# Kernel tuning notes

Measured on AMD Instinct MI355X. Metric: run time of the kernel, lower is better.

Reference implementation:

```python
import jax, jax.numpy as jnp
import numpy as np

N_NODES = 100000
N_EDGES = 1000000
IN_CH = 312
HID = 256
OUT = 256


def _sage_conv(x, src, dst, W_l, b_l, W_r, num_nodes):
    # PyG SAGEConv (mean aggr): out = mean_{j in N(i)} x_j @ W_l + b_l + x_i @ W_r
    msg = x[src]                                             # [E, C] gather
    agg = jax.ops.segment_sum(msg, dst, num_segments=num_nodes)  # [N, C]
    deg = jax.ops.segment_sum(jnp.ones((src.shape[0],), dtype=x.dtype), dst,
                              num_segments=num_nodes)        # [N]
    mean = agg / jnp.maximum(deg, 1.0)[:, None]
    return mean @ W_l + b_l + x @ W_r


def setup_inputs() -> dict:
    key = jax.random.key(0)
    ks = jax.random.split(key, 8)
    x = jax.random.normal(ks[0], (N_NODES, IN_CH), dtype=jnp.float32)
    edge_index = jax.random.randint(ks[1], (2, N_EDGES), 0, N_NODES, dtype=jnp.int64)
    s1 = 1.0 / np.sqrt(IN_CH)
    s2 = 1.0 / np.sqrt(HID)
    W1_l = jax.random.normal(ks[2], (IN_CH, HID), dtype=jnp.float32) * s1
    b1 = jnp.zeros((HID,), dtype=jnp.float32)
    W1_r = jax.random.normal(ks[3], (IN_CH, HID), dtype=jnp.float32) * s1
    W2_l = jax.random.normal(ks[4], (HID, OUT), dtype=jnp.float32) * s2
    b2 = jnp.zeros((OUT,), dtype=jnp.float32)
    W2_r = jax.random.normal(ks[5], (HID, OUT), dtype=jnp.float32) * s2
    return {"x": x, "edge_index": edge_index, "W1_l": W1_l, "b1": b1,
            "W1_r": W1_r, "W2_l": W2_l, "b2": b2, "W2_r": W2_r}


def reference(x, edge_index, W1_l, b1, W1_r, W2_l, b2, W2_r):
    src, dst = edge_index[0], edge_index[1]
    n = x.shape[0]
    h = _sage_conv(x, src, dst, W1_l, b1, W1_r, n)
    h = jax.nn.relu(h)
    out = _sage_conv(h, src, dst, W2_l, b2, W2_r, n)
    return out
```

## Files before the change

kernel.cpp:

```cpp
#include <hip/hip_runtime.h>
#include <hip/hip_bf16.h>
#include <cstdint>
#include <cstddef>

#define IN_CH 312
#define HID 256

typedef __attribute__((ext_vector_type(8))) short bf16x8;
typedef __attribute__((ext_vector_type(4))) float f32x4;
typedef __attribute__((ext_vector_type(8))) unsigned short ushort8;

__device__ __forceinline__ unsigned short f2bf(float f) {
    union { float f; unsigned u; } v; v.f = f;
    const unsigned r = v.u + 0x7FFFu + ((v.u >> 16) & 1u);
    return (unsigned short)(r >> 16);
}
__device__ __forceinline__ float bf2f(unsigned short s) {
    union { unsigned u; float f; } v; v.u = (unsigned)s << 16;
    return v.f;
}
__device__ __forceinline__ void gload_lds16(const void* g, void* l) {
    __builtin_amdgcn_global_load_lds(
        (const __attribute__((address_space(1))) void*)g,
        (__attribute__((address_space(3))) void*)l, 16, 0, 0);
}

__global__ void detect_idx_kernel(const void* __restrict__ ei, int* __restrict__ flag) {
    if (blockIdx.x == 0 && threadIdx.x == 0) {
        const int* p = (const int*)ei;
        int ok = 1;
        for (int i = 0; i < 64; ++i) ok &= (p[2 * i + 1] == 0);
        *flag = ok;
    }
}
__device__ __forceinline__ long long load_idx(const void* ei, long long i, bool is64) {
    return is64 ? ((const long long*)ei)[i] : (long long)((const int*)ei)[i];
}

__global__ void hist_kernel(const void* __restrict__ ei, const int* __restrict__ flag,
                            int* __restrict__ cnt, int E) {
    const int i = blockIdx.x * blockDim.x + threadIdx.x;
    if (i >= E) return;
    const bool is64 = (*flag != 0);
    atomicAdd(&cnt[load_idx(ei, (long long)E + i, is64)], 1);
}

__global__ void offsets_kernel(const int* __restrict__ cnt, int* __restrict__ counter,
                               int* __restrict__ beg, int* __restrict__ cur, int n) {
    const int i = blockIdx.x * blockDim.x + threadIdx.x;
    if (i >= n) return;
    const int b = atomicAdd(counter, cnt[i]);
    beg[i] = b;
    cur[i] = b;
}

__global__ void fill_kernel(const void* __restrict__ ei, const int* __restrict__ flag,
                            int* __restrict__ cur, int* __restrict__ col, int E) {
    const int i = blockIdx.x * blockDim.x + threadIdx.x;
    if (i >= E) return;
    const bool is64 = (*flag != 0);
    const long long s = load_idx(ei, i, is64);
    const long long d = load_idx(ei, (long long)E + i, is64);
    col[atomicAdd(&cur[d], 1)] = (int)s;
}

__global__ void convert_x_kernel(const float* __restrict__ x, unsigned short* __restrict__ xb,
                                 int N) {
    const int tid = blockIdx.x * blockDim.x + threadIdx.x;
    if (tid >= N * 40) return;
    const int row = tid / 40;
    const int c8 = (tid % 40) * 8;
    ushort8 o;
    if (c8 < IN_CH) {
        const float4 v0 = *(const float4*)(x + (size_t)row * IN_CH + c8);
        const float4 v1 = *(const float4*)(x + (size_t)row * IN_CH + c8 + 4);
        o[0] = f2bf(v0.x); o[1] = f2bf(v0.y); o[2] = f2bf(v0.z); o[3] = f2bf(v0.w);
        o[4] = f2bf(v1.x); o[5] = f2bf(v1.y); o[6] = f2bf(v1.z); o[7] = f2bf(v1.w);
    } else {
        o = (ushort8)0;
    }
    *(ushort8*)(xb + (size_t)row * 320 + c8) = o;
}

__global__ void convert_w_kernel(const float* __restrict__ Wl, const float* __restrict__ Wr,
                                 unsigned short* __restrict__ wt, int K, int Kpad) {
    const int tid = blockIdx.x * blockDim.x + threadIdx.x;
    if (tid >= 512 * Kpad) return;
    const int c = tid / Kpad;
    const int k = tid % Kpad;
    float v = 0.f;
    if (k < K) v = (c < 256) ? Wl[(size_t)k * 256 + c] : Wr[(size_t)k * 256 + (c - 256)];
    wt[(size_t)c * Kpad + k] = f2bf(v);
}

template <int KPAD, bool ZBF16>
__global__ __launch_bounds__(256) void mfma_gemm_kernel(
    const unsigned short* __restrict__ A,
    const unsigned short* __restrict__ WT,
    const float* __restrict__ bias,
    unsigned short* __restrict__ Y,
    void* __restrict__ Z,
    int M)
{
    __shared__ short a_lds[128 * 64];
    __shared__ short b_lds[128 * 64];

    const int lane = threadIdx.x & 63;
    const int wid  = threadIdx.x >> 6;
    const int wr = wid >> 1, wc = wid & 1;
    const int r0 = blockIdx.x * 128;
    const int c0 = blockIdx.y * 128;

    f32x4 acc[4][4];
    #pragma unroll
    for (int i = 0; i < 4; ++i)
        #pragma unroll
        for (int j = 0; j < 4; ++j) acc[i][j] = (f32x4)0.f;

    const int ldrow  = lane >> 3;
    const int schunk = (lane & 7) ^ ldrow;

    for (int kb = 0; kb < KPAD; kb += 64) {
        __syncthreads();
        #pragma unroll
        for (int j = 0; j < 4; ++j) {
            const int ld = wid * 4 + j;
            const int trow = ld * 8 + ldrow;
            const int agr = min(r0 + trow, M - 1);
            gload_lds16(A + (size_t)agr * KPAD + kb + schunk * 8,
                        (char*)a_lds + ld * 1024);
            gload_lds16(WT + (size_t)(c0 + trow) * KPAD + kb + schunk * 8,
                        (char*)b_lds + ld * 1024);
        }
        __syncthreads();

        #pragma unroll
        for (int ks = 0; ks < 2; ++ks) {
            bf16x8 af[4], bg[4];
            #pragma unroll
            for (int f = 0; f < 4; ++f) {
                const int arow = wr * 64 + f * 16 + (lane & 15);
                const int ach  = (ks * 4 + (lane >> 4)) ^ (arow & 7);
                af[f] = *(const bf16x8*)((const char*)a_lds + arow * 128 + ach * 16);
                const int brow = wc * 64 + f * 16 + (lane & 15);
                const int bch  = (ks * 4 + (lane >> 4)) ^ (brow & 7);
                bg[f] = *(const bf16x8*)((const char*)b_lds + brow * 128 + bch * 16);
            }
            #pragma unroll
            for (int fm = 0; fm < 4; ++fm)
                #pragma unroll
                for (int fn = 0; fn < 4; ++fn)
                    acc[fm][fn] = __builtin_amdgcn_mfma_f32_16x16x32_bf16(
                        af[fm], bg[fn], acc[fm][fn], 0, 0, 0);
        }
    }

    const int rbase = r0 + wr * 64 + (lane >> 4) * 4;
    const int cbase = c0 + wc * 64 + (lane & 15);
    if (c0 < 256) {
        #pragma unroll
        for (int fm = 0; fm < 4; ++fm)
            #pragma unroll
            for (int fn = 0; fn < 4; ++fn) {
                const int gc = cbase + fn * 16;
                #pragma unroll
                for (int r = 0; r < 4; ++r) {
                    const int gr = rbase + fm * 16 + r;
                    if (gr < M) Y[(size_t)gr * 256 + gc] = f2bf(acc[fm][fn][r]);
                }
            }
    } else {
        #pragma unroll
        for (int fn = 0; fn < 4; ++fn) {
            const int gc = cbase + fn * 16 - 256;
            const float bv = bias[gc];
            #pragma unroll
            for (int fm = 0; fm < 4; ++fm)
                #pragma unroll
                for (int r = 0; r < 4; ++r) {
                    const int gr = rbase + fm * 16 + r;
                    if (gr < M) {
                        const float zv = acc[fm][fn][r] + bv;
                        if (ZBF16)
                            ((unsigned short*)Z)[(size_t)gr * 256 + gc] = f2bf(zv);
                        else
                            ((float*)Z)[(size_t)gr * 256 + gc] = zv;
                    }
                }
        }
    }
}

template <bool LAYER1>
__global__ void gather_agg_kernel(const unsigned short* __restrict__ Y,
                                  const int* __restrict__ beg_arr,
                                  const int* __restrict__ cnt,
                                  const int* __restrict__ col,
                                  const void* __restrict__ Z,
                                  void* __restrict__ OUT, int N)
{
    const long long gw = ((long long)blockIdx.x * blockDim.x + threadIdx.x) >> 6;
    if (gw >= N) return;
    const int w = (int)gw;
    const int lane = threadIdx.x & 63;
    const int c4 = lane * 4;
    const int beg = beg_arr[w];
    const int deg = cnt[w];
    const int end = beg + deg;

    float4 acc = make_float4(0.f, 0.f, 0.f, 0.f);
    int e = beg;
    for (; e + 1 < end; e += 2) {
        const int s0 = col[e], s1 = col[e + 1];
        const ushort4 v0 = *(const ushort4*)(Y + (size_t)s0 * 256 + c4);
        const ushort4 v1 = *(const ushort4*)(Y + (size_t)s1 * 256 + c4);
        acc.x += bf2f(v0.x) + bf2f(v1.x);
        acc.y += bf2f(v0.y) + bf2f(v1.y);
        acc.z += bf2f(v0.z) + bf2f(v1.z);
        acc.w += bf2f(v0.w) + bf2f(v1.w);
    }
    if (e < end) {
        const ushort4 v0 = *(const ushort4*)(Y + (size_t)col[e] * 256 + c4);
        acc.x += bf2f(v0.x); acc.y += bf2f(v0.y);
        acc.z += bf2f(v0.z); acc.w += bf2f(v0.w);
    }

    const float inv = 1.0f / fmaxf((float)deg, 1.0f);
    float4 z;
    if (LAYER1) {
        const ushort4 zb = *(const ushort4*)((const unsigned short*)Z + (size_t)w * 256 + c4);
        z = make_float4(bf2f(zb.x), bf2f(zb.y), bf2f(zb.z), bf2f(zb.w));
    } else {
        z = *(const float4*)((const float*)Z + (size_t)w * 256 + c4);
    }
    float4 o;
    o.x = acc.x * inv + z.x;
    o.y = acc.y * inv + z.y;
    o.z = acc.z * inv + z.z;
    o.w = acc.w * inv + z.w;
    if (LAYER1) {
        o.x = fmaxf(o.x, 0.f); o.y = fmaxf(o.y, 0.f);
        o.z = fmaxf(o.z, 0.f); o.w = fmaxf(o.w, 0.f);
        ushort4 ob;
        ob.x = f2bf(o.x); ob.y = f2bf(o.y); ob.z = f2bf(o.z); ob.w = f2bf(o.w);
        *(ushort4*)((unsigned short*)OUT + (size_t)w * 256 + c4) = ob;
    } else {
        *(float4*)((float*)OUT + (size_t)w * 256 + c4) = o;
    }
}

extern "C" void kernel_launch(void* const* d_in, const int* in_sizes, int n_in,
                              void* d_out, int out_size, void* d_ws, size_t ws_size,
                              hipStream_t stream) {
    const float* x   = (const float*)d_in[0];
    const void*  ei  = d_in[1];
    const float* W1l = (const float*)d_in[2];
    const float* b1  = (const float*)d_in[3];
    const float* W1r = (const float*)d_in[4];
    const float* W2l = (const float*)d_in[5];
    const float* b2  = (const float*)d_in[6];
    const float* W2r = (const float*)d_in[7];

    const int N = in_sizes[0] / IN_CH;
    const int E = in_sizes[1] / 2;

    char* ws = (char*)d_ws;
    size_t off = 0;
    auto alloc = [&](size_t bytes) {
        void* p = ws + off;
        off = (off + bytes + 255) & ~(size_t)255;
        return p;
    };
    int* flag    = (int*)alloc(4);
    int* cnt     = (int*)alloc((size_t)(N + 1) * 4);
    int* counter = cnt + N;
    int* beg     = (int*)alloc((size_t)N * 4);
    int* cur     = (int*)alloc((size_t)N * 4);
    int* col     = (int*)alloc((size_t)E * 4);
    unsigned short* wt1 = (unsigned short*)alloc((size_t)512 * 320 * 2);
    unsigned short* wt2 = (unsigned short*)alloc((size_t)512 * 256 * 2);
    unsigned short* bufA = (unsigned short*)alloc((size_t)N * 320 * 2);
    unsigned short* y    = (unsigned short*)alloc((size_t)N * 256 * 2);

    float* out = (float*)d_out;
    unsigned short* z1 = (unsigned short*)d_out;

    hipMemsetAsync(cnt, 0, (size_t)(N + 1) * 4, stream);
    detect_idx_kernel<<<1, 64, 0, stream>>>(ei, flag);
    hist_kernel<<<(E + 255) / 256, 256, 0, stream>>>(ei, flag, cnt, E);
    offsets_kernel<<<(N + 255) / 256, 256, 0, stream>>>(cnt, counter, beg, cur, N);
    fill_kernel<<<(E + 255) / 256, 256, 0, stream>>>(ei, flag, cur, col, E);

    convert_x_kernel<<<(N * 40 + 255) / 256, 256, 0, stream>>>(x, bufA, N);
    convert_w_kernel<<<(512 * 320 + 255) / 256, 256, 0, stream>>>(W1l, W1r, wt1, IN_CH, 320);
    convert_w_kernel<<<(512 * 256 + 255) / 256, 256, 0, stream>>>(W2l, W2r, wt2, HID, 256);

    const dim3 ggrid((N + 127) / 128, 4);

    mfma_gemm_kernel<320, true><<<ggrid, 256, 0, stream>>>(bufA, wt1, b1, y, z1, N);
    gather_agg_kernel<true><<<(N + 3) / 4, 256, 0, stream>>>(y, beg, cnt, col, z1, bufA, N);

    mfma_gemm_kernel<256, false><<<ggrid, 256, 0, stream>>>(bufA, wt2, b2, y, out, N);
    gather_agg_kernel<false><<<(N + 3) / 4, 256, 0, stream>>>(y, beg, cnt, col, out, out, N);
}
```

Before: 535.7 us.

## Fuse fp32-to-bf16 conversion of x into GEMM and use full-width 64-row tiles

Removes the separate convert_x kernel: the first GEMM now loads fp32 x directly, converts it to bf16 in registers and writes swizzled bf16 into LDS. The GEMM tile is restructured so each block computes 64 rows by all 512 output columns, with each wave owning 128 columns. A is therefore read once instead of four times across column blocks. The trade-off is 64KB of B staged in LDS per block, more accumulators per wave (lower occupancy), and fp32 A loads that go through registers instead of direct-to-LDS loads.

```diff
diff --git a/kernel.cpp b/kernel.cpp
--- a/kernel.cpp
+++ b/kernel.cpp
@@ -8,7 +8,6 @@
 
 typedef __attribute__((ext_vector_type(8))) short bf16x8;
 typedef __attribute__((ext_vector_type(4))) float f32x4;
-typedef __attribute__((ext_vector_type(8))) unsigned short ushort8;
 
 __device__ __forceinline__ unsigned short f2bf(float f) {
     union { float f; unsigned u; } v; v.f = f;
@@ -62,24 +61,6 @@
     const long long s = load_idx(ei, i, is64);
     const long long d = load_idx(ei, (long long)E + i, is64);
     col[atomicAdd(&cur[d], 1)] = (int)s;
-}
-
-__global__ void convert_x_kernel(const float* __restrict__ x, unsigned short* __restrict__ xb,
-                                 int N) {
-    const int tid = blockIdx.x * blockDim.x + threadIdx.x;
-    if (tid >= N * 40) return;
-    const int row = tid / 40;
-    const int c8 = (tid % 40) * 8;
-    ushort8 o;
-    if (c8 < IN_CH) {
-        const float4 v0 = *(const float4*)(x + (size_t)row * IN_CH + c8);
-        const float4 v1 = *(const float4*)(x + (size_t)row * IN_CH + c8 + 4);
-        o[0] = f2bf(v0.x); o[1] = f2bf(v0.y); o[2] = f2bf(v0.z); o[3] = f2bf(v0.w);
-        o[4] = f2bf(v1.x); o[5] = f2bf(v1.y); o[6] = f2bf(v1.z); o[7] = f2bf(v1.w);
-    } else {
-        o = (ushort8)0;
-    }
-    *(ushort8*)(xb + (size_t)row * 320 + c8) = o;
 }
 
 __global__ void convert_w_kernel(const float* __restrict__ Wl, const float* __restrict__ Wr,
@@ -93,29 +74,27 @@
     wt[(size_t)c * Kpad + k] = f2bf(v);
 }
 
-template <int KPAD, bool ZBF16>
+template <int KPAD, bool AFP32, bool ZBF16>
 __global__ __launch_bounds__(256) void mfma_gemm_kernel(
-    const unsigned short* __restrict__ A,
+    const void* __restrict__ Avoid,
     const unsigned short* __restrict__ WT,
     const float* __restrict__ bias,
     unsigned short* __restrict__ Y,
     void* __restrict__ Z,
     int M)
 {
-    __shared__ short a_lds[128 * 64];
-    __shared__ short b_lds[128 * 64];
+    __shared__ short a_lds[64 * 64];
+    __shared__ short b_lds[512 * 64];
 
     const int lane = threadIdx.x & 63;
     const int wid  = threadIdx.x >> 6;
-    const int wr = wid >> 1, wc = wid & 1;
-    const int r0 = blockIdx.x * 128;
-    const int c0 = blockIdx.y * 128;
-
-    f32x4 acc[4][4];
+    const int r0   = blockIdx.x * 64;
+
+    f32x4 acc[4][8];
     #pragma unroll
     for (int i = 0; i < 4; ++i)
         #pragma unroll
-        for (int j = 0; j < 4; ++j) acc[i][j] = (f32x4)0.f;
+        for (int j = 0; j < 8; ++j) acc[i][j] = (f32x4)0.f;
 
     const int ldrow  = lane >> 3;
     const int schunk = (lane & 7) ^ ldrow;
@@ -123,46 +102,79 @@
     for (int kb = 0; kb < KPAD; kb += 64) {
         __syncthreads();
         #pragma unroll
-        for (int j = 0; j < 4; ++j) {
-            const int ld = wid * 4 + j;
+        for (int j = 0; j < 16; ++j) {
+            const int ld = wid * 16 + j;
             const int trow = ld * 8 + ldrow;
-            const int agr = min(r0 + trow, M - 1);
-            gload_lds16(A + (size_t)agr * KPAD + kb + schunk * 8,
-                        (char*)a_lds + ld * 1024);
-            gload_lds16(WT + (size_t)(c0 + trow) * KPAD + kb + schunk * 8,
+            gload_lds16(WT + (size_t)trow * KPAD + kb + schunk * 8,
                         (char*)b_lds + ld * 1024);
         }
+        if (AFP32) {
+            const float* A = (const float*)Avoid;
+            float4 v[4];
+            #pragma unroll
+            for (int it = 0; it < 4; ++it) {
+                const int idx = (int)threadIdx.x + it * 256;
+                const int row = idx >> 4, q = idx & 15;
+                const int gr = min(r0 + row, M - 1);
+                const int gk = kb + q * 4;
+                v[it] = (gk < IN_CH) ? *(const float4*)(A + (size_t)gr * IN_CH + gk)
+                                     : make_float4(0.f, 0.f, 0.f, 0.f);
+            }
+            #pragma unroll
+            for (int it = 0; it < 4; ++it) {
+                const int idx = (int)threadIdx.x + it * 256;
+                const int row = idx >> 4, q = idx & 15;
+                ushort4 b;
+                b.x = f2bf(v[it].x); b.y = f2bf(v[it].y);
+                b.z = f2bf(v[it].z); b.w = f2bf(v[it].w);
+                const int byte = row * 128 + (((q >> 1) ^ (row & 7)) * 16) + (q & 1) * 8;
+                *(ushort4*)((char*)a_lds + byte) = b;
+            }
+        } else {
+            const unsigned short* A = (const unsigned short*)Avoid;
+            #pragma unroll
+            for (int j = 0; j < 2; ++j) {
+                const int ld = wid * 2 + j;
+                const int trow = ld * 8 + ldrow;
+                const int gr = min(r0 + trow, M - 1);
+                gload_lds16(A + (size_t)gr * KPAD + kb + schunk * 8,
+                            (char*)a_lds + ld * 1024);
+            }
+        }
         __syncthreads();
 
         #pragma unroll
         for (int ks = 0; ks < 2; ++ks) {
-            bf16x8 af[4], bg[4];
+            bf16x8 af[4], bg[8];
             #pragma unroll
             for (int f = 0; f < 4; ++f) {
-                const int arow = wr * 64 + f * 16 + (lane & 15);
+                const int arow = f * 16 + (lane & 15);
                 const int ach  = (ks * 4 + (lane >> 4)) ^ (arow & 7);
                 af[f] = *(const bf16x8*)((const char*)a_lds + arow * 128 + ach * 16);
-                const int brow = wc * 64 + f * 16 + (lane & 15);
+            }
+            #pragma unroll
+            for (int f = 0; f < 8; ++f) {
+                const int brow = wid * 128 + f * 16 + (lane & 15);
                 const int bch  = (ks * 4 + (lane >> 4)) ^ (brow & 7);
                 bg[f] = *(const bf16x8*)((const char*)b_lds + brow * 128 + bch * 16);
             }
             #pragma unroll
             for (int fm = 0; fm < 4; ++fm)
                 #pragma unroll
-                for (int fn = 0; fn < 4; ++fn)
+                for (int fn = 0; fn < 8; ++fn)
                     acc[fm][fn] = __builtin_amdgcn_mfma_f32_16x16x32_bf16(
                         af[fm], bg[fn], acc[fm][fn], 0, 0, 0);
         }
     }
 
-    const int rbase = r0 + wr * 64 + (lane >> 4) * 4;
-    const int cbase = c0 + wc * 64 + (lane & 15);
-    if (c0 < 256) {
+    const int rbase = r0 + (lane >> 4) * 4;
+    const int cwave = wid * 128 + (lane & 15);
+    if (wid < 2) {
         #pragma unroll
         for (int fm = 0; fm < 4; ++fm)
             #pragma unroll
-            for (int fn = 0; fn < 4; ++fn) {
-                const int gc = cbase + fn * 16;
+            for (int fn = 0; fn < 8; ++fn) {
+                const int gc = cwave + fn * 16;
                 #pragma unroll
                 for (int r = 0; r < 4; ++r) {
                     const int gr = rbase + fm * 16 + r;
@@ -171,8 +183,8 @@
             }
     } else {
         #pragma unroll
-        for (int fn = 0; fn < 4; ++fn) {
-            const int gc = cbase + fn * 16 - 256;
+        for (int fn = 0; fn < 8; ++fn) {
+            const int gc = cwave + fn * 16 - 256;
             const float bv = bias[gc];
             #pragma unroll
             for (int fm = 0; fm < 4; ++fm)
@@ -279,8 +291,8 @@
     int* col     = (int*)alloc((size_t)E * 4);
     unsigned short* wt1 = (unsigned short*)alloc((size_t)512 * 320 * 2);
     unsigned short* wt2 = (unsigned short*)alloc((size_t)512 * 256 * 2);
-    unsigned short* bufA = (unsigned short*)alloc((size_t)N * 320 * 2);
-    unsigned short* y    = (unsigned short*)alloc((size_t)N * 256 * 2);
+    unsigned short* hb  = (unsigned short*)alloc((size_t)N * 256 * 2);
+    unsigned short* y   = (unsigned short*)alloc((size_t)N * 256 * 2);
 
     float* out = (float*)d_out;
     unsigned short* z1 = (unsigned short*)d_out;
@@ -291,15 +303,14 @@
     offsets_kernel<<<(N + 255) / 256, 256, 0, stream>>>(cnt, counter, beg, cur, N);
     fill_kernel<<<(E + 255) / 256, 256, 0, stream>>>(ei, flag, cur, col, E);
 
-    convert_x_kernel<<<(N * 40 + 255) / 256, 256, 0, stream>>>(x, bufA, N);
     convert_w_kernel<<<(512 * 320 + 255) / 256, 256, 0, stream>>>(W1l, W1r, wt1, IN_CH, 320);
     convert_w_kernel<<<(512 * 256 + 255) / 256, 256, 0, stream>>>(W2l, W2r, wt2, HID, 256);
 
-    const dim3 ggrid((N + 127) / 128, 4);
-
-    mfma_gemm_kernel<320, true><<<ggrid, 256, 0, stream>>>(bufA, wt1, b1, y, z1, N);
-    gather_agg_kernel<true><<<(N + 3) / 4, 256, 0, stream>>>(y, beg, cnt, col, z1, bufA, N);
-
-    mfma_gemm_kernel<256, false><<<ggrid, 256, 0, stream>>>(bufA, wt2, b2, y, out, N);
+    const int gblocks = (N + 63) / 64;
+
+    mfma_gemm_kernel<320, true, true><<<gblocks, 256, 0, stream>>>(x, wt1, b1, y, z1, N);
+    gather_agg_kernel<true><<<(N + 3) / 4, 256, 0, stream>>>(y, beg, cnt, col, z1, hb, N);
+
+    mfma_gemm_kernel<256, false, false><<<gblocks, 256, 0, stream>>>(hb, wt2, b2, y, out, N);
     gather_agg_kernel<false><<<(N + 3) / 4, 256, 0, stream>>>(y, beg, cnt, col, out, out, N);
 }
```

New measurement: 682.0 us. 27.3% more time.
